# Kernel optimization log

Hardware: AMD Instinct MI355X
Metric: run time of the kernel (lower is better)

Reference implementation:

```python
import jax, jax.numpy as jnp
import numpy as np

DIM = 128
N_NODES = 50000
N_EDGES = 600000
N_GRAPHS = 128
BN_EPS = 1e-5


def setup_inputs() -> dict:
    key = jax.random.key(0)
    ks = jax.random.split(key, 16)
    x = jax.random.normal(ks[0], (N_NODES, DIM), dtype=jnp.float32)
    edge_index = jax.random.randint(ks[1], (2, N_EDGES), 0, N_NODES, dtype=jnp.int64)
    edge_attr = jax.random.normal(ks[2], (N_EDGES, DIM), dtype=jnp.float32)
    u = jax.random.normal(ks[3], (N_GRAPHS, DIM), dtype=jnp.float32)
    batch = jnp.sort(jax.random.randint(ks[4], (N_NODES,), 0, N_GRAPHS, dtype=jnp.int64))
    s0 = 1.0 / np.sqrt(3 * DIM)
    s1 = 1.0 / np.sqrt(DIM)
    W0 = jax.random.uniform(ks[5], (DIM, 3 * DIM), jnp.float32, -s0, s0)
    b0 = jax.random.uniform(ks[6], (DIM,), jnp.float32, -s0, s0)
    W1 = jax.random.uniform(ks[7], (DIM, DIM), jnp.float32, -s1, s1)
    b1 = jax.random.uniform(ks[8], (DIM,), jnp.float32, -s1, s1)
    W2 = jax.random.uniform(ks[9], (DIM, DIM), jnp.float32, -s1, s1)
    b2 = jax.random.uniform(ks[10], (DIM,), jnp.float32, -s1, s1)
    g0 = jnp.ones((DIM,), jnp.float32); beta0 = jnp.zeros((DIM,), jnp.float32)
    g1 = jnp.ones((DIM,), jnp.float32); beta1 = jnp.zeros((DIM,), jnp.float32)
    g2 = jnp.ones((DIM,), jnp.float32); beta2 = jnp.zeros((DIM,), jnp.float32)
    return {"x": x, "edge_index": edge_index, "edge_attr": edge_attr, "u": u,
            "batch": batch, "W0": W0, "b0": b0, "W1": W1, "b1": b1,
            "W2": W2, "b2": b2, "g0": g0, "beta0": beta0, "g1": g1,
            "beta1": beta1, "g2": g2, "beta2": beta2}


def _bn(h, gamma, beta):
    # BatchNorm1d in training mode: biased batch statistics over axis 0
    m = h.mean(axis=0)
    v = jnp.mean((h - m) ** 2, axis=0)
    return gamma * (h - m) * jax.lax.rsqrt(v + BN_EPS) + beta


def reference(x, edge_index, edge_attr, u, batch,
              W0, b0, W1, b1, W2, b2,
              g0, beta0, g1, beta1, g2, beta2):
    n = x.shape[0]
    src = edge_index[0]
    # scatter_mean over edges -> per-node mean of incident edge features
    sums = jax.ops.segment_sum(edge_attr, src, num_segments=n)
    cnt = jax.ops.segment_sum(jnp.ones((edge_attr.shape[0],), edge_attr.dtype),
                              src, num_segments=n)
    v_e = sums / jnp.maximum(cnt, 1.0)[:, None]
    comb = jnp.concatenate([x, v_e, u[batch]], axis=1)  # [N, 3*dim]
    h = _bn(jax.nn.relu(comb @ W0.T + b0), g0, beta0)
    h = _bn(jax.nn.relu(h @ W1.T + b1), g1, beta1)
    h = _bn(jax.nn.relu(h @ W2.T + b2), g2, beta2)
    return h
```

## Files before the change

kernel.cpp:

```cpp
#include <hip/hip_runtime.h>
#include <cstddef>

#define DIMC 128
#define BN_EPS 1e-5f


__global__ void hist_kernel(const int* __restrict__ src, int* __restrict__ cnt,
                            int E) {
  int i = blockIdx.x * blockDim.x + threadIdx.x;
  const int stride = gridDim.x * blockDim.x;
  for (; i < E; i += stride) atomicAdd(&cnt[src[i]], 1);
}

__global__ void scan_pass_a(const int* __restrict__ cnt, int* __restrict__ bsums,
                            int N) {
  __shared__ int sh[256];
  const int t = threadIdx.x;
  const int idx = blockIdx.x * 256 + t;
  sh[t] = (idx < N) ? cnt[idx] : 0;
  __syncthreads();
  for (int off = 128; off > 0; off >>= 1) {
    if (t < off) sh[t] += sh[t + off];
    __syncthreads();
  }
  if (t == 0) bsums[blockIdx.x] = sh[0];
}

__global__ void scan_pass_b(int* __restrict__ bsums) {
  __shared__ int sh[256];
  const int t = threadIdx.x;
  const int v = bsums[t];
  sh[t] = v;
  __syncthreads();
  for (int off = 1; off < 256; off <<= 1) {
    const int add = (t >= off) ? sh[t - off] : 0;
    __syncthreads();
    sh[t] += add;
    __syncthreads();
  }
  bsums[t] = sh[t] - v;
}

__global__ void scan_pass_c(const int* __restrict__ cnt,
                            const int* __restrict__ bsums,
                            int* __restrict__ offs, int* __restrict__ cursor,
                            int N) {
  __shared__ int sh[256];
  const int t = threadIdx.x;
  const int idx = blockIdx.x * 256 + t;
  const int v = (idx < N) ? cnt[idx] : 0;
  sh[t] = v;
  __syncthreads();
  for (int off = 1; off < 256; off <<= 1) {
    const int add = (t >= off) ? sh[t - off] : 0;
    __syncthreads();
    sh[t] += add;
    __syncthreads();
  }
  if (idx < N) {
    const int excl = sh[t] - v + bsums[blockIdx.x];
    offs[idx] = excl;
    cursor[idx] = excl;
  }
}

__global__ void bucket_kernel(const int* __restrict__ src,
                              int* __restrict__ cursor, int* __restrict__ elist,
                              int E) {
  int i = blockIdx.x * blockDim.x + threadIdx.x;
  const int stride = gridDim.x * blockDim.x;
  for (; i < E; i += stride) {
    const int s = src[i];
    const int p = atomicAdd(&cursor[s], 1);
    elist[p] = i;
  }
}

__global__ void gather_mean_kernel(const float* __restrict__ edge_attr,
                                   const int* __restrict__ elist,
                                   const int* __restrict__ offs,
                                   const int* __restrict__ cnt,
                                   float* __restrict__ ve, int N) {
  const int wid = (blockIdx.x * blockDim.x + threadIdx.x) >> 6;
  const int lane = threadIdx.x & 63;
  if (wid >= N) return;
  const int start = offs[wid];
  const int c = cnt[wid];
  float ax = 0.f, ay = 0.f;
  int j = 0;
  for (; j + 1 < c; j += 2) {
    const int e0 = elist[start + j];
    const int e1 = elist[start + j + 1];
    const float2 a0 =
        *reinterpret_cast<const float2*>(edge_attr + (size_t)e0 * DIMC + lane * 2);
    const float2 a1 =
        *reinterpret_cast<const float2*>(edge_attr + (size_t)e1 * DIMC + lane * 2);
    ax += a0.x + a1.x;
    ay += a0.y + a1.y;
  }
  if (j < c) {
    const int e0 = elist[start + j];
    const float2 a0 =
        *reinterpret_cast<const float2*>(edge_attr + (size_t)e0 * DIMC + lane * 2);
    ax += a0.x;
    ay += a0.y;
  }
  const float inv = 1.0f / fmaxf((float)c, 1.0f);
  *reinterpret_cast<float2*>(ve + (size_t)wid * DIMC + lane * 2) =
      make_float2(ax * inv, ay * inv);
}

#define BM 64
#define BK 32

template <int KTOT, int MODE>
__launch_bounds__(256)
__global__ void gemm_bn_kernel(const float* __restrict__ A,
                               const float* __restrict__ ve,
                               const float* __restrict__ u,
                               const int* __restrict__ batch,
                               const float* __restrict__ in_scale,
                               const float* __restrict__ in_shift,
                               const float* __restrict__ W,
                               const float* __restrict__ bias,
                               float* __restrict__ H,
                               float* __restrict__ stats,
                               int N) {
  __shared__ float As[BM][BK + 4];
  __shared__ float Ws[BK][DIMC + 4];
  __shared__ float red[8][DIMC];

  const int t = threadIdx.x;
  const int row0 = blockIdx.x * BM;
  const int colb = (t & 31) * 4;
  const int rowb = (t >> 5) * 8;

  float acc[8][4];
#pragma unroll
  for (int i = 0; i < 8; ++i)
#pragma unroll
    for (int j = 0; j < 4; ++j) acc[i][j] = 0.f;

  for (int k0 = 0; k0 < KTOT; k0 += BK) {
#pragma unroll
    for (int it = 0; it < 2; ++it) {
      const int idx = t + it * 256;
      const int r = idx >> 3;
      const int kq = idx & 7;
      int grow = row0 + r;
      if (grow >= N) grow = N - 1;
      const int k = k0 + kq * 4;
      float4 v;
      if constexpr (MODE == 0) {
        if (k < 128) {
          v = *reinterpret_cast<const float4*>(A + (size_t)grow * DIMC + k);
        } else if (k < 256) {
          v = *reinterpret_cast<const float4*>(ve + (size_t)grow * DIMC + (k - 128));
        } else {
          const int g = batch[grow];
          v = *reinterpret_cast<const float4*>(u + (size_t)g * DIMC + (k - 256));
        }
      } else {
        float4 h4 = *reinterpret_cast<const float4*>(A + (size_t)grow * DIMC + k);
        float4 sc = *reinterpret_cast<const float4*>(in_scale + k);
        float4 sh = *reinterpret_cast<const float4*>(in_shift + k);
        v = make_float4(h4.x * sc.x + sh.x, h4.y * sc.y + sh.y,
                        h4.z * sc.z + sh.z, h4.w * sc.w + sh.w);
      }
      *reinterpret_cast<float4*>(&As[r][kq * 4]) = v;
    }
#pragma unroll
    for (int it = 0; it < 4; ++it) {
      const int idx = t + it * 256;
      const int c = idx >> 3;
      const int kq = idx & 7;
      float4 v = *reinterpret_cast<const float4*>(W + (size_t)c * KTOT + k0 + kq * 4);
      Ws[kq * 4 + 0][c] = v.x;
      Ws[kq * 4 + 1][c] = v.y;
      Ws[kq * 4 + 2][c] = v.z;
      Ws[kq * 4 + 3][c] = v.w;
    }
    __syncthreads();
#pragma unroll
    for (int kk0 = 0; kk0 < BK; kk0 += 4) {
      float4 a4[8];
#pragma unroll
      for (int rr = 0; rr < 8; ++rr)
        a4[rr] = *reinterpret_cast<const float4*>(&As[rowb + rr][kk0]);
#pragma unroll
      for (int q = 0; q < 4; ++q) {
        const float4 b4 = *reinterpret_cast<const float4*>(&Ws[kk0 + q][colb]);
#pragma unroll
        for (int rr = 0; rr < 8; ++rr) {
          const float av = (q == 0) ? a4[rr].x
                         : (q == 1) ? a4[rr].y
                         : (q == 2) ? a4[rr].z
                                    : a4[rr].w;
          acc[rr][0] += av * b4.x;
          acc[rr][1] += av * b4.y;
          acc[rr][2] += av * b4.z;
          acc[rr][3] += av * b4.w;
        }
      }
    }
    __syncthreads();
  }

  const float4 b4 = *reinterpret_cast<const float4*>(bias + colb);
  float s1[4] = {0.f, 0.f, 0.f, 0.f};
  float s2[4] = {0.f, 0.f, 0.f, 0.f};
#pragma unroll
  for (int rr = 0; rr < 8; ++rr) {
    const int grow = row0 + rowb + rr;
    const float v0 = fmaxf(acc[rr][0] + b4.x, 0.f);
    const float v1 = fmaxf(acc[rr][1] + b4.y, 0.f);
    const float v2 = fmaxf(acc[rr][2] + b4.z, 0.f);
    const float v3 = fmaxf(acc[rr][3] + b4.w, 0.f);
    if (grow < N) {
      *reinterpret_cast<float4*>(H + (size_t)grow * DIMC + colb) =
          make_float4(v0, v1, v2, v3);
      s1[0] += v0; s1[1] += v1; s1[2] += v2; s1[3] += v3;
      s2[0] += v0 * v0; s2[1] += v1 * v1; s2[2] += v2 * v2; s2[3] += v3 * v3;
    }
  }
  const int ty = t >> 5;
#pragma unroll
  for (int cc = 0; cc < 4; ++cc) red[ty][colb + cc] = s1[cc];
  __syncthreads();
  if (t < DIMC) {
    float s = 0.f;
#pragma unroll
    for (int r = 0; r < 8; ++r) s += red[r][t];
    atomicAdd(&stats[t], s);
  }
  __syncthreads();
#pragma unroll
  for (int cc = 0; cc < 4; ++cc) red[ty][colb + cc] = s2[cc];
  __syncthreads();
  if (t < DIMC) {
    float s = 0.f;
#pragma unroll
    for (int r = 0; r < 8; ++r) s += red[r][t];
    atomicAdd(&stats[DIMC + t], s);
  }
}

__global__ void finalize_stats_kernel(const float* __restrict__ stats,
                                      const float* __restrict__ g,
                                      const float* __restrict__ beta,
                                      float* __restrict__ scale,
                                      float* __restrict__ shift, float invN) {
  const int c = threadIdx.x;
  const float m = stats[c] * invN;
  float v = stats[DIMC + c] * invN - m * m;
  v = fmaxf(v, 0.f);
  const float sc = g[c] * rsqrtf(v + BN_EPS);
  scale[c] = sc;
  shift[c] = beta[c] - m * sc;
}

__global__ void final_affine_kernel(const float* __restrict__ h,
                                    const float* __restrict__ scale,
                                    const float* __restrict__ shift,
                                    float* __restrict__ out, int nvec4) {
  const int start = blockIdx.x * blockDim.x + threadIdx.x;
  const int stride = gridDim.x * blockDim.x;
  for (int i = start; i < nvec4; i += stride) {
    const int c = (i & 31) * 4;
    float4 hv = reinterpret_cast<const float4*>(h)[i];
    float4 sc = *reinterpret_cast<const float4*>(scale + c);
    float4 sh = *reinterpret_cast<const float4*>(shift + c);
    reinterpret_cast<float4*>(out)[i] =
        make_float4(hv.x * sc.x + sh.x, hv.y * sc.y + sh.y, hv.z * sc.z + sh.z,
                    hv.w * sc.w + sh.w);
  }
}

extern "C" void kernel_launch(void* const* d_in, const int* in_sizes, int n_in,
                              void* d_out, int out_size, void* d_ws,
                              size_t ws_size, hipStream_t stream) {
  const float* x = (const float*)d_in[0];
  const int* edge_index = (const int*)d_in[1];
  const float* edge_attr = (const float*)d_in[2];
  const float* u = (const float*)d_in[3];
  const int* batch = (const int*)d_in[4];
  const float* W0 = (const float*)d_in[5];
  const float* b0 = (const float*)d_in[6];
  const float* W1 = (const float*)d_in[7];
  const float* b1 = (const float*)d_in[8];
  const float* W2 = (const float*)d_in[9];
  const float* b2 = (const float*)d_in[10];
  const float* g0 = (const float*)d_in[11];
  const float* be0 = (const float*)d_in[12];
  const float* g1 = (const float*)d_in[13];
  const float* be1 = (const float*)d_in[14];
  const float* g2 = (const float*)d_in[15];
  const float* be2 = (const float*)d_in[16];

  const int N = in_sizes[0] / DIMC;
  const int E = in_sizes[2] / DIMC;
  const int SCAN_BLOCKS = 256;

  float* regionA = (float*)d_ws;
  float* regionB = regionA + (size_t)N * DIMC;
  int* cnt = (int*)(regionB + (size_t)N * DIMC);
  int* offs = cnt + N;
  int* cursor = offs + N + 1;
  int* elist = cursor + N;
  int* bsums = elist + E;
  float* stats = (float*)(bsums + SCAN_BLOCKS);
  float* scsh = stats + 6 * DIMC;

  float* ve = regionA;
  float* h0 = regionB;
  float* h1 = regionA;
  float* h2 = regionB;

  hipMemsetAsync(cnt, 0, N * sizeof(int), stream);
  hipMemsetAsync(stats, 0, 6 * DIMC * sizeof(float), stream);

  hist_kernel<<<512, 256, 0, stream>>>(edge_index, cnt, E);
  scan_pass_a<<<SCAN_BLOCKS, 256, 0, stream>>>(cnt, bsums, N);
  scan_pass_b<<<1, 256, 0, stream>>>(bsums);
  scan_pass_c<<<SCAN_BLOCKS, 256, 0, stream>>>(cnt, bsums, offs, cursor, N);
  bucket_kernel<<<512, 256, 0, stream>>>(edge_index, cursor, elist, E);
  gather_mean_kernel<<<(N * 64 + 255) / 256, 256, 0, stream>>>(
      edge_attr, elist, offs, cnt, ve, N);

  const int gblocks = (N + BM - 1) / BM;
  const float invN = 1.0f / (float)N;

  gemm_bn_kernel<3 * DIMC, 0><<<gblocks, 256, 0, stream>>>(
      x, ve, u, batch, nullptr, nullptr, W0, b0, h0, stats, N);
  finalize_stats_kernel<<<1, DIMC, 0, stream>>>(stats, g0, be0, scsh,
                                                scsh + DIMC, invN);

  gemm_bn_kernel<DIMC, 1><<<gblocks, 256, 0, stream>>>(
      h0, nullptr, nullptr, nullptr, scsh, scsh + DIMC, W1, b1, h1,
      stats + 2 * DIMC, N);
  finalize_stats_kernel<<<1, DIMC, 0, stream>>>(stats + 2 * DIMC, g1, be1,
                                                scsh + 2 * DIMC,
                                                scsh + 3 * DIMC, invN);

  gemm_bn_kernel<DIMC, 1><<<gblocks, 256, 0, stream>>>(
      h1, nullptr, nullptr, nullptr, scsh + 2 * DIMC, scsh + 3 * DIMC, W2, b2,
      h2, stats + 4 * DIMC, N);
  finalize_stats_kernel<<<1, DIMC, 0, stream>>>(stats + 4 * DIMC, g2, be2,
                                                scsh + 4 * DIMC,
                                                scsh + 5 * DIMC, invN);

  final_affine_kernel<<<2048, 256, 0, stream>>>(
      h2, scsh + 4 * DIMC, scsh + 5 * DIMC, (float*)d_out, (N * DIMC) / 4);
}
```

Measured before the change: 749.2 us.

## Use bf16 MFMA GEMMs, bf16 intermediates, and fold BN into next-layer weights

Replaces the fp32 SIMT GEMM with a bf16 MFMA 16x16x32 kernel that stages A and W in swizzled LDS tiles. Intermediate activations and the edge mean are now stored as bf16, which halves their memory traffic. The BatchNorm affine is folded into the next layer's weights and bias by a small kernel, so the per-element scaling is no longer done while loading A. The cost is bf16 precision loss on activations and weights, plus a few extra tiny launches.

New measurement: 663.7 us. 1.13x faster.

```diff
diff --git a/kernel.cpp b/kernel.cpp
--- a/kernel.cpp
+++ b/kernel.cpp
@@ -1,9 +1,31 @@
 #include <hip/hip_runtime.h>
+#include <hip/hip_bf16.h>
 #include <cstddef>
+#include <cstdint>
 
 #define DIMC 128
 #define BN_EPS 1e-5f
 
+typedef unsigned short u16;
+typedef short bf16x8 __attribute__((ext_vector_type(8)));
+typedef float f32x4 __attribute__((ext_vector_type(4)));
+
+__device__ inline u16 f2bf(float f) {
+  __hip_bfloat16 h = __float2bfloat16(f);
+  return __builtin_bit_cast(u16, h);
+}
+__device__ inline float bf2f(u16 u) {
+  __hip_bfloat16 h = __builtin_bit_cast(__hip_bfloat16, u);
+  return __bfloat162float(h);
+}
+__device__ inline bf16x8 pack8(const float4& a, const float4& b) {
+  bf16x8 v;
+  v[0] = (short)f2bf(a.x); v[1] = (short)f2bf(a.y);
+  v[2] = (short)f2bf(a.z); v[3] = (short)f2bf(a.w);
+  v[4] = (short)f2bf(b.x); v[5] = (short)f2bf(b.y);
+  v[6] = (short)f2bf(b.z); v[7] = (short)f2bf(b.w);
+  return v;
+}
 
 __global__ void hist_kernel(const int* __restrict__ src, int* __restrict__ cnt,
                             int E) {
@@ -80,7 +102,7 @@
                                    const int* __restrict__ elist,
                                    const int* __restrict__ offs,
                                    const int* __restrict__ cnt,
-                                   float* __restrict__ ve, int N) {
+                                   u16* __restrict__ ve, int N) {
   const int wid = (blockIdx.x * blockDim.x + threadIdx.x) >> 6;
   const int lane = threadIdx.x & 63;
   if (wid >= N) return;
@@ -106,142 +128,127 @@
     ay += a0.y;
   }
   const float inv = 1.0f / fmaxf((float)c, 1.0f);
-  *reinterpret_cast<float2*>(ve + (size_t)wid * DIMC + lane * 2) =
-      make_float2(ax * inv, ay * inv);
-}
-
-#define BM 64
-#define BK 32
+  const unsigned packed =
+      ((unsigned)f2bf(ay * inv) << 16) | (unsigned)f2bf(ax * inv);
+  reinterpret_cast<unsigned*>(ve)[(size_t)wid * 64 + lane] = packed;
+}
 
 template <int KTOT, int MODE>
-__launch_bounds__(256)
-__global__ void gemm_bn_kernel(const float* __restrict__ A,
-                               const float* __restrict__ ve,
-                               const float* __restrict__ u,
-                               const int* __restrict__ batch,
-                               const float* __restrict__ in_scale,
-                               const float* __restrict__ in_shift,
-                               const float* __restrict__ W,
-                               const float* __restrict__ bias,
-                               float* __restrict__ H,
-                               float* __restrict__ stats,
-                               int N) {
-  __shared__ float As[BM][BK + 4];
-  __shared__ float Ws[BK][DIMC + 4];
-  __shared__ float red[8][DIMC];
+__launch_bounds__(256, 2)
+__global__ void gemm_mfma_kernel(const float* __restrict__ Af32,
+                                 const u16* __restrict__ Abf,
+                                 const float* __restrict__ u,
+                                 const int* __restrict__ batch,
+                                 const float* __restrict__ W,
+                                 const float* __restrict__ bias,
+                                 u16* __restrict__ Hout,
+                                 float* __restrict__ stats,
+                                 int N) {
+  __shared__ u16 A_lds[64 * 64];
+  __shared__ u16 W_lds[128 * 64];
+  __shared__ float red[4][256];
 
   const int t = threadIdx.x;
-  const int row0 = blockIdx.x * BM;
-  const int colb = (t & 31) * 4;
-  const int rowb = (t >> 5) * 8;
-
-  float acc[8][4];
-#pragma unroll
-  for (int i = 0; i < 8; ++i)
-#pragma unroll
-    for (int j = 0; j < 4; ++j) acc[i][j] = 0.f;
-
-  for (int k0 = 0; k0 < KTOT; k0 += BK) {
+  const int w = t >> 6;
+  const int l = t & 63;
+  const int row0 = blockIdx.x * 64;
+
+  f32x4 acc[8];
+#pragma unroll
+  for (int cf = 0; cf < 8; ++cf) acc[cf] = {0.f, 0.f, 0.f, 0.f};
+
+  const int nchunk = KTOT / 64;
+  for (int ch = 0; ch < nchunk; ++ch) {
 #pragma unroll
     for (int it = 0; it < 2; ++it) {
-      const int idx = t + it * 256;
-      const int r = idx >> 3;
-      const int kq = idx & 7;
-      int grow = row0 + r;
+      const int s = t + it * 256;
+      const int row = s >> 3;
+      const int sl8 = s & 7;
+      int grow = row0 + row;
       if (grow >= N) grow = N - 1;
-      const int k = k0 + kq * 4;
-      float4 v;
+      const int kg = ch * 64 + sl8 * 8;
+      bf16x8 v;
       if constexpr (MODE == 0) {
-        if (k < 128) {
-          v = *reinterpret_cast<const float4*>(A + (size_t)grow * DIMC + k);
-        } else if (k < 256) {
-          v = *reinterpret_cast<const float4*>(ve + (size_t)grow * DIMC + (k - 128));
+        if (ch < 2) {
+          const float4* p =
+              reinterpret_cast<const float4*>(Af32 + (size_t)grow * DIMC + kg);
+          v = pack8(p[0], p[1]);
+        } else if (ch < 4) {
+          v = *reinterpret_cast<const bf16x8*>(Abf + (size_t)grow * DIMC +
+                                               (kg - 128));
         } else {
           const int g = batch[grow];
-          v = *reinterpret_cast<const float4*>(u + (size_t)g * DIMC + (k - 256));
+          const float4* p =
+              reinterpret_cast<const float4*>(u + (size_t)g * DIMC + (kg - 256));
+          v = pack8(p[0], p[1]);
         }
       } else {
-        float4 h4 = *reinterpret_cast<const float4*>(A + (size_t)grow * DIMC + k);
-        float4 sc = *reinterpret_cast<const float4*>(in_scale + k);
-        float4 sh = *reinterpret_cast<const float4*>(in_shift + k);
-        v = make_float4(h4.x * sc.x + sh.x, h4.y * sc.y + sh.y,
-                        h4.z * sc.z + sh.z, h4.w * sc.w + sh.w);
+        v = *reinterpret_cast<const bf16x8*>(Abf + (size_t)grow * DIMC + kg);
       }
-      *reinterpret_cast<float4*>(&As[r][kq * 4]) = v;
+      *reinterpret_cast<bf16x8*>(&A_lds[row * 64 + ((sl8 ^ (row & 7)) * 8)]) = v;
     }
 #pragma unroll
     for (int it = 0; it < 4; ++it) {
-      const int idx = t + it * 256;
-      const int c = idx >> 3;
-      const int kq = idx & 7;
-      float4 v = *reinterpret_cast<const float4*>(W + (size_t)c * KTOT + k0 + kq * 4);
-      Ws[kq * 4 + 0][c] = v.x;
-      Ws[kq * 4 + 1][c] = v.y;
-      Ws[kq * 4 + 2][c] = v.z;
-      Ws[kq * 4 + 3][c] = v.w;
-    }
-    __syncthreads();
-#pragma unroll
-    for (int kk0 = 0; kk0 < BK; kk0 += 4) {
-      float4 a4[8];
-#pragma unroll
-      for (int rr = 0; rr < 8; ++rr)
-        a4[rr] = *reinterpret_cast<const float4*>(&As[rowb + rr][kk0]);
-#pragma unroll
-      for (int q = 0; q < 4; ++q) {
-        const float4 b4 = *reinterpret_cast<const float4*>(&Ws[kk0 + q][colb]);
-#pragma unroll
-        for (int rr = 0; rr < 8; ++rr) {
-          const float av = (q == 0) ? a4[rr].x
-                         : (q == 1) ? a4[rr].y
-                         : (q == 2) ? a4[rr].z
-                                    : a4[rr].w;
-          acc[rr][0] += av * b4.x;
-          acc[rr][1] += av * b4.y;
-          acc[rr][2] += av * b4.z;
-          acc[rr][3] += av * b4.w;
-        }
+      const int s = t + it * 256;
+      const int o = s >> 3;
+      const int sl8 = s & 7;
+      const float4* p =
+          reinterpret_cast<const float4*>(W + (size_t)o * KTOT + ch * 64 + sl8 * 8);
+      bf16x8 v = pack8(p[0], p[1]);
+      *reinterpret_cast<bf16x8*>(&W_lds[o * 64 + ((sl8 ^ (o & 7)) * 8)]) = v;
+    }
+    __syncthreads();
+#pragma unroll
+    for (int ks = 0; ks < 2; ++ks) {
+      const int arow = w * 16 + (l & 15);
+      const int asl = ks * 4 + (l >> 4);
+      const bf16x8 af = *reinterpret_cast<const bf16x8*>(
+          &A_lds[arow * 64 + ((asl ^ (arow & 7)) * 8)]);
+#pragma unroll
+      for (int cf = 0; cf < 8; ++cf) {
+        const int o = cf * 16 + (l & 15);
+        const bf16x8 bfv = *reinterpret_cast<const bf16x8*>(
+            &W_lds[o * 64 + ((asl ^ (o & 7)) * 8)]);
+        acc[cf] =
+            __builtin_amdgcn_mfma_f32_16x16x32_bf16(af, bfv, acc[cf], 0, 0, 0);
       }
     }
     __syncthreads();
   }
 
-  const float4 b4 = *reinterpret_cast<const float4*>(bias + colb);
-  float s1[4] = {0.f, 0.f, 0.f, 0.f};
-  float s2[4] = {0.f, 0.f, 0.f, 0.f};
-#pragma unroll
-  for (int rr = 0; rr < 8; ++rr) {
-    const int grow = row0 + rowb + rr;
-    const float v0 = fmaxf(acc[rr][0] + b4.x, 0.f);
-    const float v1 = fmaxf(acc[rr][1] + b4.y, 0.f);
-    const float v2 = fmaxf(acc[rr][2] + b4.z, 0.f);
-    const float v3 = fmaxf(acc[rr][3] + b4.w, 0.f);
-    if (grow < N) {
-      *reinterpret_cast<float4*>(H + (size_t)grow * DIMC + colb) =
-          make_float4(v0, v1, v2, v3);
-      s1[0] += v0; s1[1] += v1; s1[2] += v2; s1[3] += v3;
-      s2[0] += v0 * v0; s2[1] += v1 * v1; s2[2] += v2 * v2; s2[3] += v3 * v3;
-    }
-  }
-  const int ty = t >> 5;
-#pragma unroll
-  for (int cc = 0; cc < 4; ++cc) red[ty][colb + cc] = s1[cc];
-  __syncthreads();
-  if (t < DIMC) {
-    float s = 0.f;
-#pragma unroll
-    for (int r = 0; r < 8; ++r) s += red[r][t];
-    atomicAdd(&stats[t], s);
-  }
-  __syncthreads();
-#pragma unroll
-  for (int cc = 0; cc < 4; ++cc) red[ty][colb + cc] = s2[cc];
-  __syncthreads();
-  if (t < DIMC) {
-    float s = 0.f;
-#pragma unroll
-    for (int r = 0; r < 8; ++r) s += red[r][t];
-    atomicAdd(&stats[DIMC + t], s);
+  const int cbase = l & 15;
+  const int rgrp = l >> 4;
+#pragma unroll
+  for (int cf = 0; cf < 8; ++cf) {
+    const int col = cf * 16 + cbase;
+    const float bv = bias[col];
+    float s1 = 0.f, s2 = 0.f;
+#pragma unroll
+    for (int r = 0; r < 4; ++r) {
+      const int grow = row0 + w * 16 + rgrp * 4 + r;
+      const float vv = fmaxf(acc[cf][r] + bv, 0.f);
+      if (grow < N) {
+        Hout[(size_t)grow * DIMC + col] = f2bf(vv);
+        s1 += vv;
+        s2 += vv * vv;
+      }
+    }
+    s1 += __shfl_xor(s1, 16, 64);
+    s1 += __shfl_xor(s1, 32, 64);
+    s2 += __shfl_xor(s2, 16, 64);
+    s2 += __shfl_xor(s2, 32, 64);
+    if (l < 16) {
+      red[w][col] = s1;
+      red[w][128 + col] = s2;
+    }
+  }
+  __syncthreads();
+  if (t < 128) {
+    const float a = red[0][t] + red[1][t] + red[2][t] + red[3][t];
+    const float b =
+        red[0][128 + t] + red[1][128 + t] + red[2][128 + t] + red[3][128 + t];
+    atomicAdd(&stats[t], a);
+    atomicAdd(&stats[DIMC + t], b);
   }
 }
 
@@ -259,20 +266,39 @@
   shift[c] = beta[c] - m * sc;
 }
 
-__global__ void final_affine_kernel(const float* __restrict__ h,
+__global__ void fold_bn_kernel(const float* __restrict__ W,
+                               const float* __restrict__ b,
+                               const float* __restrict__ scale,
+                               const float* __restrict__ shift,
+                               float* __restrict__ Wp, float* __restrict__ bp) {
+  __shared__ float sh[128];
+  const int o = blockIdx.x;
+  const int k = threadIdx.x;
+  const float wv = W[(size_t)o * DIMC + k];
+  Wp[(size_t)o * DIMC + k] = wv * scale[k];
+  sh[k] = wv * shift[k];
+  __syncthreads();
+  for (int off = 64; off > 0; off >>= 1) {
+    if (k < off) sh[k] += sh[k + off];
+    __syncthreads();
+  }
+  if (k == 0) bp[o] = b[o] + sh[0];
+}
+
+__global__ void final_affine_kernel(const u16* __restrict__ h,
                                     const float* __restrict__ scale,
                                     const float* __restrict__ shift,
                                     float* __restrict__ out, int nvec4) {
-  const int start = blockIdx.x * blockDim.x + threadIdx.x;
+  int i = blockIdx.x * blockDim.x + threadIdx.x;
   const int stride = gridDim.x * blockDim.x;
-  for (int i = start; i < nvec4; i += stride) {
+  for (; i < nvec4; i += stride) {
     const int c = (i & 31) * 4;
-    float4 hv = reinterpret_cast<const float4*>(h)[i];
-    float4 sc = *reinterpret_cast<const float4*>(scale + c);
-    float4 sh = *reinterpret_cast<const float4*>(shift + c);
+    const ushort4 hv = reinterpret_cast<const ushort4*>(h)[i];
+    const float4 sc = *reinterpret_cast<const float4*>(scale + c);
+    const float4 sh = *reinterpret_cast<const float4*>(shift + c);
     reinterpret_cast<float4*>(out)[i] =
-        make_float4(hv.x * sc.x + sh.x, hv.y * sc.y + sh.y, hv.z * sc.z + sh.z,
-                    hv.w * sc.w + sh.w);
+        make_float4(bf2f(hv.x) * sc.x + sh.x, bf2f(hv.y) * sc.y + sh.y,
+                    bf2f(hv.z) * sc.z + sh.z, bf2f(hv.w) * sc.w + sh.w);
   }
 }
 
@@ -281,8 +307,8 @@
                               size_t ws_size, hipStream_t stream) {
   const float* x = (const float*)d_in[0];
   const int* edge_index = (const int*)d_in[1];
+  const float* u = (const float*)d_in[3];
   const float* edge_attr = (const float*)d_in[2];
-  const float* u = (const float*)d_in[3];
   const int* batch = (const int*)d_in[4];
   const float* W0 = (const float*)d_in[5];
   const float* b0 = (const float*)d_in[6];
@@ -301,20 +327,28 @@
   const int E = in_sizes[2] / DIMC;
   const int SCAN_BLOCKS = 256;
 
-  float* regionA = (float*)d_ws;
-  float* regionB = regionA + (size_t)N * DIMC;
-  int* cnt = (int*)(regionB + (size_t)N * DIMC);
-  int* offs = cnt + N;
-  int* cursor = offs + N + 1;
-  int* elist = cursor + N;
-  int* bsums = elist + E;
-  float* stats = (float*)(bsums + SCAN_BLOCKS);
-  float* scsh = stats + 6 * DIMC;
-
-  float* ve = regionA;
-  float* h0 = regionB;
-  float* h1 = regionA;
-  float* h2 = regionB;
+  uintptr_t p = (uintptr_t)d_ws;
+  auto take = [&p](size_t bytes) {
+    p = (p + 63) & ~(uintptr_t)63;
+    uintptr_t r = p;
+    p += bytes;
+    return r;
+  };
+  u16* ve = (u16*)take((size_t)N * DIMC * 2);
+  u16* h0 = (u16*)take((size_t)N * DIMC * 2);
+  u16* h1 = (u16*)take((size_t)N * DIMC * 2);
+  u16* h2 = (u16*)take((size_t)N * DIMC * 2);
+  int* cnt = (int*)take((size_t)N * 4);
+  int* offs = (int*)take((size_t)(N + 1) * 4);
+  int* cursor = (int*)take((size_t)N * 4);
+  int* elist = (int*)take((size_t)E * 4);
+  int* bsums = (int*)take((size_t)SCAN_BLOCKS * 4);
+  float* stats = (float*)take(6 * DIMC * 4);
+  float* scsh = (float*)take(6 * DIMC * 4);
+  float* W1p = (float*)take((size_t)DIMC * DIMC * 4);
+  float* b1p = (float*)take(DIMC * 4);
+  float* W2p = (float*)take((size_t)DIMC * DIMC * 4);
+  float* b2p = (float*)take(DIMC * 4);
 
   hipMemsetAsync(cnt, 0, N * sizeof(int), stream);
   hipMemsetAsync(stats, 0, 6 * DIMC * sizeof(float), stream);
@@ -327,24 +361,26 @@
   gather_mean_kernel<<<(N * 64 + 255) / 256, 256, 0, stream>>>(
       edge_attr, elist, offs, cnt, ve, N);
 
-  const int gblocks = (N + BM - 1) / BM;
+  const int gblocks = (N + 63) / 64;
   const float invN = 1.0f / (float)N;
 
-  gemm_bn_kernel<3 * DIMC, 0><<<gblocks, 256, 0, stream>>>(
-      x, ve, u, batch, nullptr, nullptr, W0, b0, h0, stats, N);
+  gemm_mfma_kernel<3 * DIMC, 0><<<gblocks, 256, 0, stream>>>(
+      x, ve, u, batch, W0, b0, h0, stats, N);
   finalize_stats_kernel<<<1, DIMC, 0, stream>>>(stats, g0, be0, scsh,
                                                 scsh + DIMC, invN);
-
-  gemm_bn_kernel<DIMC, 1><<<gblocks, 256, 0, stream>>>(
-      h0, nullptr, nullptr, nullptr, scsh, scsh + DIMC, W1, b1, h1,
-      stats + 2 * DIMC, N);
+  fold_bn_kernel<<<DIMC, DIMC, 0, stream>>>(W1, b1, scsh, scsh + DIMC, W1p,
+                                            b1p);
+
+  gemm_mfma_kernel<DIMC, 1><<<gblocks, 256, 0, stream>>>(
+      nullptr, h0, nullptr, nullptr, W1p, b1p, h1, stats + 2 * DIMC, N);
   finalize_stats_kernel<<<1, DIMC, 0, stream>>>(stats + 2 * DIMC, g1, be1,
                                                 scsh + 2 * DIMC,
                                                 scsh + 3 * DIMC, invN);
-
-  gemm_bn_kernel<DIMC, 1><<<gblocks, 256, 0, stream>>>(
-      h1, nullptr, nullptr, nullptr, scsh + 2 * DIMC, scsh + 3 * DIMC, W2, b2,
-      h2, stats + 4 * DIMC, N);
+  fold_bn_kernel<<<DIMC, DIMC, 0, stream>>>(W2, b2, scsh + 2 * DIMC,
+                                            scsh + 3 * DIMC, W2p, b2p);
+
+  gemm_mfma_kernel<DIMC, 1><<<gblocks, 256, 0, stream>>>(
+      nullptr, h1, nullptr, nullptr, W2p, b2p, h2, stats + 4 * DIMC, N);
   finalize_stats_kernel<<<1, DIMC, 0, stream>>>(stats + 4 * DIMC, g2, be2,
                                                 scsh + 4 * DIMC,
                                                 scsh + 5 * DIMC, invN);
```
